# Kernel tuning notes

Hardware: AMD Instinct MI355X
Metric: run time of the kernel (lower is better)

Reference implementation:

```python
import jax, jax.numpy as jnp
import numpy as np

H, W = 256, 256
N = 512
EPS = 1e-4


def setup_inputs() -> dict:
    key = jax.random.key(0)
    k1, k2, k3, k4 = jax.random.split(key, 4)
    means3D = jax.random.normal(k1, (N, 3), dtype=jnp.float32) * 2.0
    # PSD 3D covariances with ~few-pixel projected footprint
    A = jax.random.normal(k2, (N, 3, 3), dtype=jnp.float32) * 0.1
    covs3d = A @ jnp.swapaxes(A, -1, -2)
    colors = jax.random.uniform(k3, (N, 3), dtype=jnp.float32)
    opacities = jax.random.uniform(k4, (N,), dtype=jnp.float32)
    K = jnp.array([[300.0, 0.0, W / 2.0], [0.0, 300.0, H / 2.0], [0.0, 0.0, 1.0]], dtype=jnp.float32)
    R = jnp.eye(3, dtype=jnp.float32)
    t = jnp.array([0.0, 0.0, 10.0], dtype=jnp.float32)
    return dict(means3D=means3D, covs3d=covs3d, colors=colors, opacities=opacities, K=K, R=R, t=t)


def reference(means3D, covs3d, colors, opacities, K, R, t):
    dtype = means3D.dtype
    # --- projection ---
    cam = means3D @ R.T + t[None, :]            # (N,3)
    z = cam[:, 2]
    depths = jnp.clip(z, 1.0)                   # clamp(min=1.0)
    screen = cam @ K.T
    means2D = screen[:, :2] / screen[:, 2:3]    # (N,2)
    fx, fy = K[0, 0], K[1, 1]
    zero = jnp.zeros_like(z)
    # Jacobian rows (row 2 is all zeros, as in the original)
    J = jnp.stack([
        jnp.stack([fx / z, zero, -(fx * cam[:, 0]) / (z * z)], axis=-1),
        jnp.stack([zero, fy / z, -(fy * cam[:, 1]) / (z * z)], axis=-1),
        jnp.stack([zero, zero, zero], axis=-1),
    ], axis=1)                                   # (N,3,3)
    covs_cam = jnp.einsum('ij,njk,lk->nil', R, covs3d, R)       # R Sigma R^T
    covs2D = jnp.einsum('nki,nkl,nlj->nij', J, covs_cam, J)[:, :2, :2]  # J^T Sigma_cam J, top-left 2x2
    valid = (depths > 1.0) & (depths < 50.0)
    # --- depth sort ---
    order = jnp.argsort(depths)
    means2D = means2D[order]
    covs2D = covs2D[order]
    colors_s = colors[order]
    op_s = opacities[order]
    valid = valid[order]
    # --- per-Gaussian pixel evaluation ---
    yy, xx = jnp.meshgrid(jnp.arange(H, dtype=dtype), jnp.arange(W, dtype=dtype), indexing='ij')
    pixels = jnp.stack([xx, yy], axis=-1)                        # (H,W,2)
    dx = pixels[None] - means2D[:, None, None, :]                # (N,H,W,2)
    c = covs2D + EPS * jnp.eye(2, dtype=dtype)
    a, b = c[:, 0, 0], c[:, 0, 1]
    cc, d = c[:, 1, 0], c[:, 1, 1]
    det = a * d - b * cc                                          # (N,)
    inv = jnp.stack([jnp.stack([d, -b], -1), jnp.stack([-cc, a], -1)], axis=1) / det[:, None, None]
    dxi = jnp.einsum('nhwi,nij->nhwj', dx, inv)
    mahal = jnp.sum(dxi * dx, axis=-1)                            # (N,H,W)
    norm = 1.0 / (2.0 * jnp.pi * jnp.sqrt(det))
    gauss = norm[:, None, None] * jnp.exp(-0.5 * mahal)
    gauss = gauss * valid.astype(dtype)[:, None, None]
    # --- front-to-back alpha compositing ---
    alphas = op_s[:, None, None] * gauss                          # (N,H,W)
    T = jnp.cumprod(jnp.concatenate([jnp.ones((1, H, W), dtype=dtype), 1.0 - alphas[:-1]], axis=0), axis=0)
    weights = alphas * T
    rendered = jnp.einsum('nhw,nc->hwc', weights, colors_s)       # (H,W,3)
    return rendered
```

## Files before the change

kernel.cpp:

```cpp
#include <hip/hip_runtime.h>
#include <math.h>

#define IMG_H 256
#define IMG_W 256
#define EPSV 1e-4f
#define SEGS 8
#define PIX_PER_BLK 64
#define SKIP_EPS 1e-7f

struct __align__(16) GData {
    float4 h0, h1, h2;
};

__global__ __launch_bounds__(1024)
void GaussianRenderer_preprocess(const float* __restrict__ means3D,
                                 const float* __restrict__ covs3d,
                                 const float* __restrict__ colors,
                                 const float* __restrict__ opac,
                                 const float* __restrict__ Km,
                                 const float* __restrict__ Rm,
                                 const float* __restrict__ tv,
                                 GData* __restrict__ out, int N)
{
    __shared__ float sdepth[1024];
    const int i = threadIdx.x;

    const float R00=Rm[0], R01=Rm[1], R02=Rm[2];
    const float R10=Rm[3], R11=Rm[4], R12=Rm[5];
    const float R20=Rm[6], R21=Rm[7], R22=Rm[8];
    const float K00=Km[0], K01=Km[1], K02=Km[2];
    const float K10=Km[3], K11=Km[4], K12=Km[5];
    const float K20=Km[6], K21=Km[7], K22=Km[8];
    const float fx=Km[0], fy=Km[4];
    const float t0=tv[0], t1=tv[1], t2=tv[2];

    float depth = 0.0f;
    GData gd = {};

    if (i < N) {
        const float m0 = means3D[i*3+0], m1 = means3D[i*3+1], m2 = means3D[i*3+2];
        const float c0 = R00*m0 + R01*m1 + R02*m2 + t0;
        const float c1 = R10*m0 + R11*m1 + R12*m2 + t1;
        const float c2 = R20*m0 + R21*m1 + R22*m2 + t2;
        const float z = c2;
        depth = fmaxf(z, 1.0f);

        const float s0 = K00*c0 + K01*c1 + K02*c2;
        const float s1 = K10*c0 + K11*c1 + K12*c2;
        const float s2 = K20*c0 + K21*c1 + K22*c2;
        const float mx = s0 / s2, my = s1 / s2;

        const float* C = covs3d + i*9;
        const float C00=C[0],C01=C[1],C02=C[2],C10=C[3],C11=C[4],C12=C[5],C20=C[6],C21=C[7],C22=C[8];
        const float M00 = R00*C00 + R01*C10 + R02*C20;
        const float M01 = R00*C01 + R01*C11 + R02*C21;
        const float M02 = R00*C02 + R01*C12 + R02*C22;
        const float M10 = R10*C00 + R11*C10 + R12*C20;
        const float M11 = R10*C01 + R11*C11 + R12*C21;
        const float M12 = R10*C02 + R11*C12 + R12*C22;
        const float S00 = M00*R00 + M01*R01 + M02*R02;
        const float S01 = M00*R10 + M01*R11 + M02*R12;
        const float S10 = M10*R00 + M11*R01 + M12*R02;
        const float S11 = M10*R10 + M11*R11 + M12*R12;

        const float j0 = fx / z, j1 = fy / z;
        const float a  = j0*j0*S00 + EPSV;
        const float b  = j0*S01*j1;
        const float cc = j1*S10*j0;
        const float d  = j1*j1*S11 + EPSV;

        const float det    = a*d - b*cc;
        const float invdet = 1.0f / det;
        const float norm   = 0.15915494309189535f / sqrtf(det);
        const bool valid   = (depth > 1.0f) && (depth < 50.0f);
        const float coeff  = valid ? (opac[i] * norm) : 0.0f;

        float rx2 = -1.0f, ry2 = -1.0f;
        if (coeff > SKIP_EPS) {
            const float L = __logf(coeff * (1.0f / SKIP_EPS));
            rx2 = 2.0f * a * L;
            ry2 = 2.0f * d * L;
        }

        gd.h0 = make_float4(mx, my, rx2, ry2);
        gd.h1 = make_float4(-0.5f * d * invdet,
                             0.5f * (b + cc) * invdet,
                            -0.5f * a * invdet,
                            coeff);
        gd.h2 = make_float4(colors[i*3+0], colors[i*3+1], colors[i*3+2], 0.f);
    }

    sdepth[i] = depth;
    __syncthreads();

    if (i < N) {
        int rank = 0;
        const int n4 = N >> 2;
        const float4* sd4 = (const float4*)sdepth;
        for (int j4 = 0; j4 < n4; ++j4) {
            const float4 v = sd4[j4];
            const int j = j4 * 4;
            rank += (v.x < depth || (v.x == depth && (j + 0) < i)) ? 1 : 0;
            rank += (v.y < depth || (v.y == depth && (j + 1) < i)) ? 1 : 0;
            rank += (v.z < depth || (v.z == depth && (j + 2) < i)) ? 1 : 0;
            rank += (v.w < depth || (v.w == depth && (j + 3) < i)) ? 1 : 0;
        }
        for (int j = n4 * 4; j < N; ++j) {
            const float dj = sdepth[j];
            rank += (dj < depth || (dj == depth && j < i)) ? 1 : 0;
        }
        out[rank] = gd;
    }
}

__device__ __forceinline__ float rlane(float v, int n) {
    return __int_as_float(__builtin_amdgcn_readlane(__float_as_int(v), n));
}

__global__ __launch_bounds__(512)
void GaussianRenderer_render(const GData* __restrict__ g,
                             float* __restrict__ out, int N)
{
    const int seg  = __builtin_amdgcn_readfirstlane(threadIdx.x >> 6);
    const int lane = threadIdx.x & 63;
    const int p    = blockIdx.x * PIX_PER_BLK + lane;
    const float px = (float)(p & (IMG_W - 1));
    const float py = (float)(p >> 8);
    const float cx = (float)((blockIdx.x * PIX_PER_BLK) & (IMG_W - 1)) + 31.5f;

    const int segLen = (N + SEGS - 1) / SEGS;
    const int gBeg = seg * segLen;
    const int gEnd = (gBeg + segLen < N) ? (gBeg + segLen) : N;

    float T = 1.0f, ar = 0.0f, ag = 0.0f, ab = 0.0f;

    for (int base = gBeg; base < gEnd; base += 64) {
        const int idx = base + lane;
        float4 h0 = make_float4(0.f, 0.f, -1.f, -1.f), h1 = h0, h2 = h0;
        if (idx < gEnd) {
            const GData gd = g[idx];
            h0 = gd.h0; h1 = gd.h1; h2 = gd.h2;
        }
        const float dxm = fmaxf(fabsf(h0.x - cx) - 31.5f, 0.0f);
        const float dym = py - h0.y;
        const bool hit = (dxm * dxm <= h0.z) && (dym * dym <= h0.w);

        unsigned long long m = __ballot(hit);
        while (m) {
            const int n = __builtin_ctzll(m);
            m &= m - 1;
            const float mx = rlane(h0.x, n), my = rlane(h0.y, n);
            const float qa = rlane(h1.x, n), qb = rlane(h1.y, n);
            const float qc = rlane(h1.z, n), co = rlane(h1.w, n);
            const float cr = rlane(h2.x, n), cg = rlane(h2.y, n);
            const float cb = rlane(h2.z, n);

            const float dx = px - mx;
            const float dy = py - my;
            const float q  = (qa*dx + qb*dy)*dx + qc*(dy*dy);
            const float alpha = co * __expf(q);
            const float w = alpha * T;
            ar += w * cr;
            ag += w * cg;
            ab += w * cb;
            T  -= w;
        }
    }

    __shared__ float4 part[SEGS][PIX_PER_BLK];
    part[seg][lane] = make_float4(ar, ag, ab, T);
    __syncthreads();

    if (seg == 0) {
        float Tp = 1.0f, r = 0.0f, gg = 0.0f, b = 0.0f;
        #pragma unroll
        for (int s = 0; s < SEGS; ++s) {
            const float4 v = part[s][lane];
            r  += Tp * v.x;
            gg += Tp * v.y;
            b  += Tp * v.z;
            Tp *= v.w;
        }
        out[p*3 + 0] = r;
        out[p*3 + 1] = gg;
        out[p*3 + 2] = b;
    }
}

extern "C" void kernel_launch(void* const* d_in, const int* in_sizes, int n_in,
                              void* d_out, int out_size, void* d_ws, size_t ws_size,
                              hipStream_t stream)
{
    const float* means3D = (const float*)d_in[0];
    const float* covs3d  = (const float*)d_in[1];
    const float* colors  = (const float*)d_in[2];
    const float* opac    = (const float*)d_in[3];
    const float* Km      = (const float*)d_in[4];
    const float* Rm      = (const float*)d_in[5];
    const float* tv      = (const float*)d_in[6];
    const int N = in_sizes[3];

    GData* gbuf = (GData*)d_ws;

    int threads = ((N + 63) / 64) * 64;
    if (threads > 1024) threads = 1024;
    GaussianRenderer_preprocess<<<1, threads, 0, stream>>>(
        means3D, covs3d, colors, opac, Km, Rm, tv, gbuf, N);

    const int total = IMG_H * IMG_W;
    GaussianRenderer_render<<<(total + PIX_PER_BLK - 1) / PIX_PER_BLK, 512, 0, stream>>>(
        gbuf, (float*)d_out, N);
}
```

Before: 85.37 us.

## Parallelize preprocess rank sort across multiple blocks with split comparisons

Preprocessing previously ran as a single block where each thread serially compared its depth against all N depths. Now N/64 blocks each recompute all depths into shared memory. Eight threads share each Gaussian's rank count and the partial counts are summed. This spreads the O(N^2) rank computation over many CUs to shorten the serial preprocess latency, at the cost of redundant depth computation per block. It also adds padding with infinity and supports N up to 2048.

Measured after the change: 74.14 us. 13.2% less time.

```diff
diff --git a/kernel.cpp b/kernel.cpp
--- a/kernel.cpp
+++ b/kernel.cpp
@@ -7,12 +7,14 @@
 #define SEGS 8
 #define PIX_PER_BLK 64
 #define SKIP_EPS 1e-7f
+#define GPB 64
+#define MAXN 2048
 
 struct __align__(16) GData {
     float4 h0, h1, h2;
 };
 
-__global__ __launch_bounds__(1024)
+__global__ __launch_bounds__(512)
 void GaussianRenderer_preprocess(const float* __restrict__ means3D,
                                  const float* __restrict__ covs3d,
                                  const float* __restrict__ colors,
@@ -22,28 +24,70 @@
                                  const float* __restrict__ tv,
                                  GData* __restrict__ out, int N)
 {
-    __shared__ float sdepth[1024];
-    const int i = threadIdx.x;
+    __shared__ __align__(16) float sdepth[MAXN + 4];
+    __shared__ int srank[512];
 
     const float R00=Rm[0], R01=Rm[1], R02=Rm[2];
     const float R10=Rm[3], R11=Rm[4], R12=Rm[5];
     const float R20=Rm[6], R21=Rm[7], R22=Rm[8];
-    const float K00=Km[0], K01=Km[1], K02=Km[2];
-    const float K10=Km[3], K11=Km[4], K12=Km[5];
-    const float K20=Km[6], K21=Km[7], K22=Km[8];
-    const float fx=Km[0], fy=Km[4];
-    const float t0=tv[0], t1=tv[1], t2=tv[2];
-
-    float depth = 0.0f;
-    GData gd = {};
-
-    if (i < N) {
+    const float t2=tv[2];
+
+    const int Npad = (N + 3) & ~3;
+
+    for (int i = threadIdx.x; i < Npad; i += 512) {
+        float depth = __builtin_inff();
+        if (i < N) {
+            const float m0 = means3D[i*3+0], m1 = means3D[i*3+1], m2 = means3D[i*3+2];
+            const float z = R20*m0 + R21*m1 + R22*m2 + t2;
+            depth = fmaxf(z, 1.0f);
+        }
+        sdepth[i] = depth;
+    }
+    __syncthreads();
+
+    {
+        const int g   = blockIdx.x * GPB + (threadIdx.x >> 3);
+        const int sub = threadIdx.x & 7;
+        int rank = 0;
+        if (g < N) {
+            const float depth = sdepth[g];
+            const int total4  = Npad >> 2;
+            const int chunk4  = (total4 + 7) >> 3;
+            const int b4 = sub * chunk4;
+            const int e4 = (b4 + chunk4 < total4) ? (b4 + chunk4) : total4;
+            const float4* sd4 = (const float4*)sdepth;
+            for (int j4 = b4; j4 < e4; ++j4) {
+                const float4 v = sd4[j4];
+                const int j = j4 * 4;
+                rank += (v.x < depth || (v.x == depth && (j + 0) < g)) ? 1 : 0;
+                rank += (v.y < depth || (v.y == depth && (j + 1) < g)) ? 1 : 0;
+                rank += (v.z < depth || (v.z == depth && (j + 2) < g)) ? 1 : 0;
+                rank += (v.w < depth || (v.w == depth && (j + 3) < g)) ? 1 : 0;
+            }
+        }
+        srank[threadIdx.x] = rank;
+    }
+    __syncthreads();
+
+    const int t = threadIdx.x;
+    const int i = blockIdx.x * GPB + t;
+    if (t < GPB && i < N) {
+        int rank = 0;
+        #pragma unroll
+        for (int s = 0; s < 8; ++s) rank += srank[t*8 + s];
+
+        const float K00=Km[0], K01=Km[1], K02=Km[2];
+        const float K10=Km[3], K11=Km[4], K12=Km[5];
+        const float K20=Km[6], K21=Km[7], K22=Km[8];
+        const float fx=Km[0], fy=Km[4];
+        const float t0=tv[0], t1=tv[1];
+
         const float m0 = means3D[i*3+0], m1 = means3D[i*3+1], m2 = means3D[i*3+2];
         const float c0 = R00*m0 + R01*m1 + R02*m2 + t0;
         const float c1 = R10*m0 + R11*m1 + R12*m2 + t1;
         const float c2 = R20*m0 + R21*m1 + R22*m2 + t2;
         const float z = c2;
-        depth = fmaxf(z, 1.0f);
+        const float depth = fmaxf(z, 1.0f);
 
         const float s0 = K00*c0 + K01*c1 + K02*c2;
         const float s1 = K10*c0 + K11*c1 + K12*c2;
@@ -82,33 +126,13 @@
             ry2 = 2.0f * d * L;
         }
 
+        GData gd;
         gd.h0 = make_float4(mx, my, rx2, ry2);
         gd.h1 = make_float4(-0.5f * d * invdet,
                              0.5f * (b + cc) * invdet,
                             -0.5f * a * invdet,
                             coeff);
         gd.h2 = make_float4(colors[i*3+0], colors[i*3+1], colors[i*3+2], 0.f);
-    }
-
-    sdepth[i] = depth;
-    __syncthreads();
-
-    if (i < N) {
-        int rank = 0;
-        const int n4 = N >> 2;
-        const float4* sd4 = (const float4*)sdepth;
-        for (int j4 = 0; j4 < n4; ++j4) {
-            const float4 v = sd4[j4];
-            const int j = j4 * 4;
-            rank += (v.x < depth || (v.x == depth && (j + 0) < i)) ? 1 : 0;
-            rank += (v.y < depth || (v.y == depth && (j + 1) < i)) ? 1 : 0;
-            rank += (v.z < depth || (v.z == depth && (j + 2) < i)) ? 1 : 0;
-            rank += (v.w < depth || (v.w == depth && (j + 3) < i)) ? 1 : 0;
-        }
-        for (int j = n4 * 4; j < N; ++j) {
-            const float dj = sdepth[j];
-            rank += (dj < depth || (dj == depth && j < i)) ? 1 : 0;
-        }
         out[rank] = gd;
     }
 }
@@ -202,9 +226,8 @@
 
     GData* gbuf = (GData*)d_ws;
 
-    int threads = ((N + 63) / 64) * 64;
-    if (threads > 1024) threads = 1024;
-    GaussianRenderer_preprocess<<<1, threads, 0, stream>>>(
+    const int preBlocks = (N + GPB - 1) / GPB;
+    GaussianRenderer_preprocess<<<preBlocks, 512, 0, stream>>>(
         means3D, covs3d, colors, opac, Km, Rm, tv, gbuf, N);
 
     const int total = IMG_H * IMG_W;
```
